# Kernel optimization log

Hardware: AMD Instinct MI355X
Metric: run time of the kernel (lower is better)

Reference implementation:

```python
import jax, jax.numpy as jnp
import numpy as np

D_MODEL = 1024
N_HEADS = 16
D_HEAD = D_MODEL // N_HEADS
ROPE_BASE = 10000.0


def setup_inputs() -> dict:
    key = jax.random.key(0)
    k1, k2, k3, k4, k5 = jax.random.split(key, 5)
    std = 0.02 / np.sqrt(2 * 12)  # scaled_xavier with n_layers=12
    x = jax.random.normal(k1, (2, 2048, D_MODEL), dtype=jnp.float32)
    qkv_w = jax.random.normal(k2, (3 * D_MODEL, D_MODEL), dtype=jnp.float32) * std
    qkv_b = jnp.zeros((3 * D_MODEL,), dtype=jnp.float32)
    proj_w = jax.random.normal(k3, (D_MODEL, D_MODEL), dtype=jnp.float32) * std
    proj_b = jnp.zeros((D_MODEL,), dtype=jnp.float32)
    return {"x": x, "qkv_w": qkv_w, "qkv_b": qkv_b, "proj_w": proj_w, "proj_b": proj_b}


def _rope_cos_sin(seq_len, dtype):
    inv_freq = 1.0 / (ROPE_BASE ** (jnp.arange(0, D_HEAD, 2, dtype=jnp.float32) / D_HEAD))
    t = jnp.arange(seq_len, dtype=jnp.float32)
    freqs = jnp.einsum("t,d->td", t, inv_freq)          # [S, Dh/2]
    freqs = jnp.concatenate([freqs, freqs], axis=-1)      # [S, Dh]
    return jnp.cos(freqs).astype(dtype), jnp.sin(freqs).astype(dtype)


def _rotate_half(x):
    x1, x2 = jnp.split(x, 2, axis=-1)
    return jnp.concatenate([-x2, x1], axis=-1)


def reference(x, qkv_w, qkv_b, proj_w, proj_b):
    B, S, D = x.shape
    H, Dh = N_HEADS, D_HEAD
    scale = 1.0 / np.sqrt(Dh)

    qkv = x @ qkv_w.T + qkv_b                              # [B, S, 3D]
    qkv = qkv.reshape(B, S, 3, H, Dh)
    q = jnp.transpose(qkv[:, :, 0], (0, 2, 1, 3))          # [B, H, S, Dh]
    k = jnp.transpose(qkv[:, :, 1], (0, 2, 1, 3))
    v = jnp.transpose(qkv[:, :, 2], (0, 2, 1, 3))

    cos, sin = _rope_cos_sin(S, x.dtype)                   # [S, Dh]
    q = q * cos + _rotate_half(q) * sin
    k = k * cos + _rotate_half(k) * sin

    scores = jnp.einsum("bhsd,bhtd->bhst", q, k) * scale   # [B, H, S, S]
    causal = jnp.triu(jnp.ones((S, S), dtype=bool), k=1)
    neg = jnp.finfo(scores.dtype).min
    scores = jnp.where(causal[None, None], neg, scores)

    probs = jax.nn.softmax(scores, axis=-1)
    ctx = jnp.einsum("bhst,bhtd->bhsd", probs, v)          # [B, H, S, Dh]
    out = jnp.transpose(ctx, (0, 2, 1, 3)).reshape(B, S, D)
    out = out @ proj_w.T + proj_b
    return out
```

## Files before the change

kernel.cpp:

```cpp
#include <hip/hip_runtime.h>
#include <hip/hip_bf16.h>

#define BATCH 2
#define SEQ   2048
#define DMODEL 1024
#define NHEADS 16
#define DHEAD  64
#define MTOT   (BATCH * SEQ)
#define QKSTR  2048

typedef __attribute__((ext_vector_type(8))) short bf16x8;
typedef __attribute__((ext_vector_type(4))) float f32x4;

__device__ __forceinline__ void glds16(const void* g, void* l)
{
    __builtin_amdgcn_global_load_lds(
        (const __attribute__((address_space(1))) unsigned int*)g,
        (__attribute__((address_space(3))) unsigned int*)l, 16, 0, 0);
}

__device__ __forceinline__ unsigned cvt_pk_bf16(float lo, float hi)
{
    unsigned r;
    asm("v_cvt_pk_bf16_f32 %0, %1, %2" : "=v"(r) : "v"(lo), "v"(hi));
    return r;
}

__global__ void cast_all_kernel(
    const float* __restrict__ a, __hip_bfloat16* __restrict__ oa, int na4,
    const float* __restrict__ b, __hip_bfloat16* __restrict__ ob, int nb4,
    const float* __restrict__ c, __hip_bfloat16* __restrict__ oc, int nc4)
{
    int i = blockIdx.x * blockDim.x + threadIdx.x;
    const float* src; __hip_bfloat16* dst; int j = i;
    if (j < na4) { src = a; dst = oa; }
    else {
        j -= na4;
        if (j < nb4) { src = b; dst = ob; }
        else {
            j -= nb4;
            if (j >= nc4) return;
            src = c; dst = oc;
        }
    }
    float4 v = ((const float4*)src)[j];
    __hip_bfloat16 tmp[4];
    tmp[0] = __float2bfloat16(v.x);
    tmp[1] = __float2bfloat16(v.y);
    tmp[2] = __float2bfloat16(v.z);
    tmp[3] = __float2bfloat16(v.w);
    *(uint2*)(dst + 4 * (size_t)j) = *(const uint2*)tmp;
}

#define GBK 64

__device__ __forceinline__ void store_out(float* p, float v) { *p = v; }
__device__ __forceinline__ void store_out(__hip_bfloat16* p, float v) { *p = __float2bfloat16(v); }

template <typename OutT, int MODE, int TM, int TN, int MINW>
__global__ __launch_bounds__(256, MINW) void gemm_bias_kernel(
    const __hip_bfloat16* __restrict__ A, const __hip_bfloat16* __restrict__ W,
    const float* __restrict__ bias, OutT* __restrict__ out,
    __hip_bfloat16* __restrict__ vtg,
    int M, int N, int K)
{
    const int MI = TM / 32;
    const int NI = TN / 32;
    const int bm = blockIdx.x * TM;
    const int bn = blockIdx.y * TN;
    const int tid = threadIdx.x;
    const int wave = tid >> 6;
    const int lane = tid & 63;
    const int quad = lane >> 4;
    const int l16 = lane & 15;
    const int wm = (wave & 1) * (TM / 2);
    const int wn = (wave >> 1) * (TN / 2);

    __shared__ __hip_bfloat16 As[TM * GBK];
    __shared__ __hip_bfloat16 Bs[TN * GBK];

    f32x4 acc[MI][NI] = {};

    const int srow = lane >> 3;
    const int gc8 = (((lane & 7) ^ srow)) * 8;

    for (int kt = 0; kt < K; kt += GBK) {
#pragma unroll
        for (int t = 0; t < MI; t++) {
            int i = wave * MI + t;
            glds16(A + (size_t)(bm + i * 8 + srow) * K + kt + gc8, As + i * 512);
        }
#pragma unroll
        for (int t = 0; t < NI; t++) {
            int i = wave * NI + t;
            glds16(W + (size_t)(bn + i * 8 + srow) * K + kt + gc8, Bs + i * 512);
        }
        __syncthreads();

#pragma unroll
        for (int kk = 0; kk < 2; kk++) {
            bf16x8 af[MI], bfr[NI];
#pragma unroll
            for (int i = 0; i < MI; i++) {
                int ra = wm + i * 16 + l16;
                af[i] = *(const bf16x8*)(As + ra * 64 + (((kk << 2) + quad) ^ (ra & 7)) * 8);
            }
#pragma unroll
            for (int i = 0; i < NI; i++) {
                int rb = wn + i * 16 + l16;
                bfr[i] = *(const bf16x8*)(Bs + rb * 64 + (((kk << 2) + quad) ^ (rb & 7)) * 8);
            }
#pragma unroll
            for (int mi = 0; mi < MI; mi++)
#pragma unroll
                for (int ni = 0; ni < NI; ni++)
                    acc[mi][ni] = __builtin_amdgcn_mfma_f32_16x16x32_bf16(
                        af[mi], bfr[ni], acc[mi][ni], 0, 0, 0);
        }
        __syncthreads();
    }

    if (MODE == 1 && (bn + wn) < 2 * DMODEL) {
#pragma unroll
        for (int ni = 0; ni < 2; ni++) {
            int col = bn + wn + ni * 16 + l16;
            int i32 = col & 31;
            float invf = exp2f(-13.287712379549449f * (float)i32 * (1.0f / 32.0f));
            float b1 = bias[col], b2 = bias[col + 32];
#pragma unroll
            for (int mi = 0; mi < MI; mi++) {
#pragma unroll
                for (int r = 0; r < 4; r++) {
                    int row = bm + wm + mi * 16 + quad * 4 + r;
                    int s = row & (SEQ - 1);
                    float ang = (float)s * invf;
                    float sn, cs;
                    __sincosf(ang, &sn, &cs);
                    float x1 = acc[mi][ni][r] + b1;
                    float x2 = acc[mi][ni + 2][r] + b2;
                    store_out(&out[(size_t)row * QKSTR + col], x1 * cs - x2 * sn);
                    store_out(&out[(size_t)row * QKSTR + col + 32], x2 * cs + x1 * sn);
                }
            }
        }
    } else if (MODE == 1) {
#pragma unroll
        for (int ni = 0; ni < NI; ni++) {
            int colg = bn + wn + ni * 16 + l16;
            int vcol = colg - 2 * DMODEL;
            int hh = vcol >> 6, dh = vcol & 63;
            float bv = bias[colg];
#pragma unroll
            for (int mi = 0; mi < MI; mi++) {
                int row0 = bm + wm + mi * 16 + quad * 4;
                int bb = row0 >> 11;
                int ss = row0 & (SEQ - 1);
                __hip_bfloat16 tmp[4];
#pragma unroll
                for (int r = 0; r < 4; r++)
                    tmp[r] = __float2bfloat16(acc[mi][ni][r] + bv);
                *(uint2*)(vtg + (((size_t)bb * NHEADS + hh) * DHEAD + dh) * SEQ + ss) =
                    *(uint2*)tmp;
            }
        }
    } else {
#pragma unroll
        for (int mi = 0; mi < MI; mi++)
#pragma unroll
            for (int ni = 0; ni < NI; ni++) {
                int col = bn + wn + ni * 16 + l16;
                float bv = bias[col];
#pragma unroll
                for (int r = 0; r < 4; r++) {
                    int row = bm + wm + mi * 16 + quad * 4 + r;
                    store_out(&out[(size_t)row * N + col], acc[mi][ni][r] + bv);
                }
            }
    }
}

__global__ __launch_bounds__(256, 4) void flash_attn_mfma_kernel(
    const __hip_bfloat16* __restrict__ qkb,
    const __hip_bfloat16* __restrict__ vtg,
    __hip_bfloat16* __restrict__ ctx)
{
    const int bh = blockIdx.x;
    const int b = bh >> 4, h = bh & 15;
    const int qt = 31 - blockIdx.y;
    const int tid = threadIdx.x;
    const int w = tid >> 6;
    const int lane = tid & 63;
    const int quad = lane >> 4;
    const int l16 = lane & 15;

    __shared__ alignas(16) __hip_bfloat16 Ks[2][64 * 64];
    __shared__ alignas(16) __hip_bfloat16 Vt[2][64 * 64];
    __shared__ alignas(16) __hip_bfloat16 Ps[64 * 64];

    const __hip_bfloat16* qbase = qkb + (size_t)b * SEQ * QKSTR + h * DHEAD;
    const __hip_bfloat16* kbase = qbase + DMODEL;
    const __hip_bfloat16* vbase = vtg + (size_t)bh * DHEAD * SEQ;

    const __hip_bfloat16* qrow = qbase + (size_t)(qt * 64 + w * 16 + l16) * QKSTR;
    bf16x8 qf0 = *(const bf16x8*)(qrow + quad * 8);
    bf16x8 qf1 = *(const bf16x8*)(qrow + 32 + quad * 8);

    const int srow = lane >> 3;
    const int gc8 = ((lane & 7) ^ srow) * 8;
    const __hip_bfloat16* kg = kbase + (size_t)(w * 16 + srow) * QKSTR + gc8;
    const __hip_bfloat16* vg = vbase + (size_t)(w * 16 + srow) * SEQ + gc8;

    const int xr = l16 & 7;
    const int fo0 = l16 * 64 + ((quad ^ xr) << 3);
    const int fo1 = l16 * 64 + (((4 + quad) ^ xr) << 3);
    const int pband = w * 16;
    char* const psb = (char*)Ps;
    const int pr0 = (pband + l16) * 128 + ((quad ^ xr) << 4);
    const int pr1 = (pband + l16) * 128 + (((4 + quad) ^ xr) << 4);
    int pwc[4];
#pragma unroll
    for (int nt = 0; nt < 4; nt++)
        pwc[nt] = (pband + l16) * 128 +
                  ((((nt << 1) + (quad >> 1)) ^ xr) << 4) + (quad & 1) * 8;

    const short onev = (l16 == 0) ? (short)0x3F80 : (short)0;
    const bf16x8 ones = {onev, onev, onev, onev, onev, onev, onev, onev};

    f32x4 oacc[5] = {};

    auto stage = [&](int t, int buf) {
        const __hip_bfloat16* kt_ = kg + (size_t)t * 64 * QKSTR;
        const __hip_bfloat16* vt_ = vg + t * 64;
        glds16(kt_,              &Ks[buf][w * 1024]);
        glds16(kt_ + 8 * QKSTR,  &Ks[buf][w * 1024 + 512]);
        glds16(vt_,              &Vt[buf][w * 1024]);
        glds16(vt_ + 8 * SEQ,    &Vt[buf][w * 1024 + 512]);
    };

    stage(0, 0);

    for (int jt = 0; jt <= qt; jt++) {
        __syncthreads();
        const int cur = jt & 1;
        if (jt < qt) stage(jt + 1, cur ^ 1);
        const __hip_bfloat16* ks = Ks[cur];
        const __hip_bfloat16* vs = Vt[cur];

        f32x4 s4[4] = {};
        __builtin_amdgcn_s_setprio(1);
#pragma unroll
        for (int nt = 0; nt < 4; nt++)
            s4[nt] = __builtin_amdgcn_mfma_f32_16x16x32_bf16(
                *(const bf16x8*)(ks + nt * 1024 + fo0), qf0, s4[nt], 0, 0, 0);
#pragma unroll
        for (int nt = 0; nt < 4; nt++)
            s4[nt] = __builtin_amdgcn_mfma_f32_16x16x32_bf16(
                *(const bf16x8*)(ks + nt * 1024 + fo1), qf1, s4[nt], 0, 0, 0);
        __builtin_amdgcn_s_setprio(0);

        const bool diag = (jt == qt);
        const int qq = w * 16 + l16;
#pragma unroll
        for (int nt = 0; nt < 4; nt++) {
            float p0 = exp2f(s4[nt][0] * 0.1803368801f);
            float p1 = exp2f(s4[nt][1] * 0.1803368801f);
            float p2 = exp2f(s4[nt][2] * 0.1803368801f);
            float p3 = exp2f(s4[nt][3] * 0.1803368801f);
            if (diag) {
                int k0 = nt * 16 + quad * 4;
                p0 = (k0 + 0 <= qq) ? p0 : 0.f;
                p1 = (k0 + 1 <= qq) ? p1 : 0.f;
                p2 = (k0 + 2 <= qq) ? p2 : 0.f;
                p3 = (k0 + 3 <= qq) ? p3 : 0.f;
            }
            uint2 pv;
            pv.x = cvt_pk_bf16(p0, p1);
            pv.y = cvt_pk_bf16(p2, p3);
            *(uint2*)(psb + pwc[nt]) = pv;
        }

        bf16x8 pf0 = *(const bf16x8*)(psb + pr0);
        bf16x8 pf1 = *(const bf16x8*)(psb + pr1);
        __builtin_amdgcn_s_setprio(1);
#pragma unroll
        for (int dt = 0; dt < 4; dt++)
            oacc[dt] = __builtin_amdgcn_mfma_f32_16x16x32_bf16(
                pf0, *(const bf16x8*)(vs + dt * 1024 + fo0), oacc[dt], 0, 0, 0);
        oacc[4] = __builtin_amdgcn_mfma_f32_16x16x32_bf16(pf0, ones, oacc[4], 0, 0, 0);
#pragma unroll
        for (int dt = 0; dt < 4; dt++)
            oacc[dt] = __builtin_amdgcn_mfma_f32_16x16x32_bf16(
                pf1, *(const bf16x8*)(vs + dt * 1024 + fo1), oacc[dt], 0, 0, 0);
        oacc[4] = __builtin_amdgcn_mfma_f32_16x16x32_bf16(pf1, ones, oacc[4], 0, 0, 0);
        __builtin_amdgcn_s_setprio(0);
    }

#pragma unroll
    for (int r = 0; r < 4; r++) {
        float lv = __shfl(oacc[4][r], lane & 48);
        float il = 1.0f / lv;
        int qg = qt * 64 + w * 16 + quad * 4 + r;
        __hip_bfloat16* op = ctx + (((size_t)b * SEQ + qg) * NHEADS + h) * DHEAD + l16;
#pragma unroll
        for (int dt = 0; dt < 4; dt++)
            op[dt * 16] = __float2bfloat16(oacc[dt][r] * il);
    }
}

extern "C" void kernel_launch(void* const* d_in, const int* in_sizes, int n_in,
                              void* d_out, int out_size, void* d_ws, size_t ws_size,
                              hipStream_t stream)
{
    const float* x      = (const float*)d_in[0];
    const float* qkv_w  = (const float*)d_in[1];
    const float* qkv_b  = (const float*)d_in[2];
    const float* proj_w = (const float*)d_in[3];
    const float* proj_b = (const float*)d_in[4];
    float* out = (float*)d_out;

    char* w = (char*)d_ws;
    __hip_bfloat16* qkb = (__hip_bfloat16*)w;  w += (size_t)MTOT * QKSTR * 2;
    __hip_bfloat16* vtg = (__hip_bfloat16*)w;  w += (size_t)MTOT * DMODEL * 2;
    __hip_bfloat16* ctx = (__hip_bfloat16*)w;  w += (size_t)MTOT * DMODEL * 2;
    __hip_bfloat16* xb  = (__hip_bfloat16*)w;  w += (size_t)MTOT * DMODEL * 2;
    __hip_bfloat16* wqk = (__hip_bfloat16*)w;  w += (size_t)3 * DMODEL * DMODEL * 2;
    __hip_bfloat16* wpr = (__hip_bfloat16*)w;

    const int na4 = MTOT * DMODEL / 4;
    const int nb4 = 3 * DMODEL * DMODEL / 4;
    const int nc4 = DMODEL * DMODEL / 4;

    cast_all_kernel<<<(na4 + nb4 + nc4 + 255) / 256, 256, 0, stream>>>(
        x, xb, na4, qkv_w, wqk, nb4, proj_w, wpr, nc4);

    gemm_bias_kernel<__hip_bfloat16, 1, 128, 128, 3>
        <<<dim3(MTOT / 128, (3 * DMODEL) / 128), 256, 0, stream>>>(
        xb, wqk, qkv_b, qkb, vtg, MTOT, 3 * DMODEL, DMODEL);

    flash_attn_mfma_kernel<<<dim3(BATCH * NHEADS, 32), 256, 0, stream>>>(qkb, vtg, ctx);

    gemm_bias_kernel<float, 0, 64, 128, 6>
        <<<dim3(MTOT / 64, DMODEL / 128), 256, 0, stream>>>(
        ctx, wpr, proj_b, out, nullptr, MTOT, DMODEL, DMODEL);
}
```

Before: 168.6 us.

## Balance causal attention work by pairing query tiles and splitting keys

Each attention block now does a fixed 16–17 key-tile iterations instead of 1–32. A role-0 block handles a short query tile qa and then the first part of a long tile qb. A role-1 block handles the rest of qb. The partial unnormalized outputs and row sums for the long tiles go to fp32 scratch buffers, and a new finalize kernel combines them. This removes the causal load imbalance and tail effect, at the cost of an extra kernel launch and extra global traffic for the fp32 partials. The o0 buffer reuses the xb workspace, which is safe only because xb is no longer needed after the QKV GEMM.

```diff
diff --git a/kernel.cpp b/kernel.cpp
--- a/kernel.cpp
+++ b/kernel.cpp
@@ -182,11 +182,16 @@
 __global__ __launch_bounds__(256, 4) void flash_attn_mfma_kernel(
     const __hip_bfloat16* __restrict__ qkb,
     const __hip_bfloat16* __restrict__ vtg,
-    __hip_bfloat16* __restrict__ ctx)
+    __hip_bfloat16* __restrict__ ctx,
+    float* __restrict__ o0, float* __restrict__ o1,
+    float* __restrict__ l0, float* __restrict__ l1)
 {
     const int bh = blockIdx.x;
     const int b = bh >> 4, h = bh & 15;
-    const int qt = 31 - blockIdx.y;
+    const int yy = blockIdx.y;
+    const int role = yy >> 4;
+    const int y = yy & 15;
+    const int qa = y, qb = 31 - y;
     const int tid = threadIdx.x;
     const int w = tid >> 6;
     const int lane = tid & 63;
@@ -201,9 +206,13 @@
     const __hip_bfloat16* kbase = qbase + DMODEL;
     const __hip_bfloat16* vbase = vtg + (size_t)bh * DHEAD * SEQ;
 
-    const __hip_bfloat16* qrow = qbase + (size_t)(qt * 64 + w * 16 + l16) * QKSTR;
+    const int qt0 = role ? qb : qa;
+    const __hip_bfloat16* qrow = qbase + (size_t)(qt0 * 64 + w * 16 + l16) * QKSTR;
     bf16x8 qf0 = *(const bf16x8*)(qrow + quad * 8);
     bf16x8 qf1 = *(const bf16x8*)(qrow + 32 + quad * 8);
+    const __hip_bfloat16* qrows = qbase + (size_t)(qb * 64 + w * 16 + l16) * QKSTR;
+    bf16x8 qs0 = *(const bf16x8*)(qrows + quad * 8);
+    bf16x8 qs1 = *(const bf16x8*)(qrows + 32 + quad * 8);
 
     const int srow = lane >> 3;
     const int gc8 = ((lane & 7) ^ srow) * 8;
@@ -237,12 +246,28 @@
         glds16(vt_ + 8 * SEQ,    &Vt[buf][w * 1024 + 512]);
     };
 
-    stage(0, 0);
-
-    for (int jt = 0; jt <= qt; jt++) {
+    auto kof = [&](int n) { return role ? n : (n <= qa ? n : n + 15 - qa); };
+
+    auto write_ctx = [&](int qt) {
+#pragma unroll
+        for (int r = 0; r < 4; r++) {
+            float lv = __shfl(oacc[4][r], lane & 48);
+            float il = 1.0f / lv;
+            int qg = qt * 64 + w * 16 + quad * 4 + r;
+            __hip_bfloat16* op = ctx + (((size_t)b * SEQ + qg) * NHEADS + h) * DHEAD + l16;
+#pragma unroll
+            for (int dt = 0; dt < 4; dt++)
+                op[dt * 16] = __float2bfloat16(oacc[dt][r] * il);
+        }
+    };
+
+    const int nit = 17 - role;
+    stage(kof(0), 0);
+
+    for (int n = 0; n < nit; n++) {
         __syncthreads();
-        const int cur = jt & 1;
-        if (jt < qt) stage(jt + 1, cur ^ 1);
+        const int cur = n & 1;
+        if (n + 1 < nit) stage(kof(n + 1), cur ^ 1);
         const __hip_bfloat16* ks = Ks[cur];
         const __hip_bfloat16* vs = Vt[cur];
 
@@ -258,7 +283,7 @@
                 *(const bf16x8*)(ks + nt * 1024 + fo1), qf1, s4[nt], 0, 0, 0);
         __builtin_amdgcn_s_setprio(0);
 
-        const bool diag = (jt == qt);
+        const bool diag = (!role) && (n == qa || n == 16);
         const int qq = w * 16 + l16;
 #pragma unroll
         for (int nt = 0; nt < 4; nt++) {
@@ -293,18 +318,50 @@
                 pf1, *(const bf16x8*)(vs + dt * 1024 + fo1), oacc[dt], 0, 0, 0);
         oacc[4] = __builtin_amdgcn_mfma_f32_16x16x32_bf16(pf1, ones, oacc[4], 0, 0, 0);
         __builtin_amdgcn_s_setprio(0);
+
+        if (!role && n == qa) {
+            write_ctx(qa);
+#pragma unroll
+            for (int i = 0; i < 5; i++) oacc[i] = f32x4{0.f, 0.f, 0.f, 0.f};
+            qf0 = qs0; qf1 = qs1;
+        }
     }
 
+    float* ob = role ? o1 : o0;
+    float* lb = role ? l1 : l0;
+    const int rbase = bh * 1024 + (qb - 16) * 64 + w * 16;
 #pragma unroll
     for (int r = 0; r < 4; r++) {
-        float lv = __shfl(oacc[4][r], lane & 48);
-        float il = 1.0f / lv;
-        int qg = qt * 64 + w * 16 + quad * 4 + r;
-        __hip_bfloat16* op = ctx + (((size_t)b * SEQ + qg) * NHEADS + h) * DHEAD + l16;
+        int rr = rbase + quad * 4 + r;
 #pragma unroll
         for (int dt = 0; dt < 4; dt++)
-            op[dt * 16] = __float2bfloat16(oacc[dt][r] * il);
+            ob[(size_t)rr * 64 + dt * 16 + l16] = oacc[dt][r];
+        if (l16 == 0) lb[rr] = oacc[4][r];
     }
+}
+
+__global__ void attn_finalize_kernel(
+    const float* __restrict__ o0, const float* __restrict__ o1,
+    const float* __restrict__ l0, const float* __restrict__ l1,
+    __hip_bfloat16* __restrict__ ctx)
+{
+    int t = blockIdx.x * blockDim.x + threadIdx.x;
+    int dh4 = t & 15;
+    int row = t >> 4;
+    int bh = row >> 10;
+    int qrow = row & 1023;
+    int b = bh >> 4, h = bh & 15;
+    float il = 1.0f / (l0[row] + l1[row]);
+    float4 a = ((const float4*)(o0 + (size_t)row * 64))[dh4];
+    float4 c = ((const float4*)(o1 + (size_t)row * 64))[dh4];
+    __hip_bfloat16 tmp[4];
+    tmp[0] = __float2bfloat16((a.x + c.x) * il);
+    tmp[1] = __float2bfloat16((a.y + c.y) * il);
+    tmp[2] = __float2bfloat16((a.z + c.z) * il);
+    tmp[3] = __float2bfloat16((a.w + c.w) * il);
+    int s = 1024 + qrow;
+    *(uint2*)(ctx + (((size_t)b * SEQ + s) * NHEADS + h) * DHEAD + dh4 * 4) =
+        *(uint2*)tmp;
 }
 
 extern "C" void kernel_launch(void* const* d_in, const int* in_sizes, int n_in,
@@ -324,7 +381,11 @@
     __hip_bfloat16* ctx = (__hip_bfloat16*)w;  w += (size_t)MTOT * DMODEL * 2;
     __hip_bfloat16* xb  = (__hip_bfloat16*)w;  w += (size_t)MTOT * DMODEL * 2;
     __hip_bfloat16* wqk = (__hip_bfloat16*)w;  w += (size_t)3 * DMODEL * DMODEL * 2;
-    __hip_bfloat16* wpr = (__hip_bfloat16*)w;
+    __hip_bfloat16* wpr = (__hip_bfloat16*)w;  w += (size_t)DMODEL * DMODEL * 2;
+    float* o0 = (float*)xb;
+    float* o1 = (float*)w;  w += (size_t)32 * 1024 * 64 * 4;
+    float* l0 = (float*)w;  w += (size_t)32 * 1024 * 4;
+    float* l1 = (float*)w;
 
     const int na4 = MTOT * DMODEL / 4;
     const int nb4 = 3 * DMODEL * DMODEL / 4;
@@ -337,7 +398,10 @@
         <<<dim3(MTOT / 128, (3 * DMODEL) / 128), 256, 0, stream>>>(
         xb, wqk, qkv_b, qkb, vtg, MTOT, 3 * DMODEL, DMODEL);
 
-    flash_attn_mfma_kernel<<<dim3(BATCH * NHEADS, 32), 256, 0, stream>>>(qkb, vtg, ctx);
+    flash_attn_mfma_kernel<<<dim3(BATCH * NHEADS, 32), 256, 0, stream>>>(
+        qkb, vtg, ctx, o0, o1, l0, l1);
+
+    attn_finalize_kernel<<<2048, 256, 0, stream>>>(o0, o1, l0, l1, ctx);
 
     gemm_bias_kernel<float, 0, 64, 128, 6>
         <<<dim3(MTOT / 64, DMODEL / 128), 256, 0, stream>>>(
```

Measured after the change: 176.1 us. 1.04x slower.

## Feed softmax probabilities directly into 16x16x16 MFMA, drop LDS P staging

Applied to the files above, without the earlier changes.

Removes the shared-memory round trip for the probability tile. The S accumulator layout of each 16-column block is reused directly as the A operand of the 16x16x16 bf16 MFMA, reading V fragments with matching swizzled offsets. Dropping the Ps buffer frees LDS, so launch bounds are raised to 5 blocks per CU. Query tiles are also reordered to interleave long and short causal tiles for better load balance. The trade is twice as many smaller MFMAs for the PV product and possibly more register pressure under the tighter occupancy bound.

```diff
diff --git a/kernel.cpp b/kernel.cpp
--- a/kernel.cpp
+++ b/kernel.cpp
@@ -10,6 +10,7 @@
 #define QKSTR  2048
 
 typedef __attribute__((ext_vector_type(8))) short bf16x8;
+typedef __attribute__((ext_vector_type(4))) short bf16x4;
 typedef __attribute__((ext_vector_type(4))) float f32x4;
 
 __device__ __forceinline__ void glds16(const void* g, void* l)
@@ -179,14 +180,15 @@
     }
 }
 
-__global__ __launch_bounds__(256, 4) void flash_attn_mfma_kernel(
+__global__ __launch_bounds__(256, 5) void flash_attn_mfma_kernel(
     const __hip_bfloat16* __restrict__ qkb,
     const __hip_bfloat16* __restrict__ vtg,
     __hip_bfloat16* __restrict__ ctx)
 {
     const int bh = blockIdx.x;
     const int b = bh >> 4, h = bh & 15;
-    const int qt = 31 - blockIdx.y;
+    const int y = blockIdx.y;
+    const int qt = (y < 8) ? 31 - y : (y < 16) ? y - 8 : (y < 24) ? 39 - y : y - 16;
     const int tid = threadIdx.x;
     const int w = tid >> 6;
     const int lane = tid & 63;
@@ -195,7 +197,6 @@
 
     __shared__ alignas(16) __hip_bfloat16 Ks[2][64 * 64];
     __shared__ alignas(16) __hip_bfloat16 Vt[2][64 * 64];
-    __shared__ alignas(16) __hip_bfloat16 Ps[64 * 64];
 
     const __hip_bfloat16* qbase = qkb + (size_t)b * SEQ * QKSTR + h * DHEAD;
     const __hip_bfloat16* kbase = qbase + DMODEL;
@@ -213,18 +214,16 @@
     const int xr = l16 & 7;
     const int fo0 = l16 * 64 + ((quad ^ xr) << 3);
     const int fo1 = l16 * 64 + (((4 + quad) ^ xr) << 3);
-    const int pband = w * 16;
-    char* const psb = (char*)Ps;
-    const int pr0 = (pband + l16) * 128 + ((quad ^ xr) << 4);
-    const int pr1 = (pband + l16) * 128 + (((4 + quad) ^ xr) << 4);
-    int pwc[4];
+    int vbse[4], vchk[4];
+#pragma unroll
+    for (int dt = 0; dt < 4; dt++)
+        vbse[dt] = (dt * 16 + l16) * 64 + (quad & 1) * 4;
 #pragma unroll
     for (int nt = 0; nt < 4; nt++)
-        pwc[nt] = (pband + l16) * 128 +
-                  ((((nt << 1) + (quad >> 1)) ^ xr) << 4) + (quad & 1) * 8;
-
-    const short onev = (l16 == 0) ? (short)0x3F80 : (short)0;
-    const bf16x8 ones = {onev, onev, onev, onev, onev, onev, onev, onev};
+        vchk[nt] = (((nt << 1) + (quad >> 1)) ^ xr) << 3;
+
+    const short ov = (l16 == 0) ? (short)0x3F80 : (short)0;
+    const bf16x4 ones4 = {ov, ov, ov, ov};
 
     f32x4 oacc[5] = {};
 
@@ -273,26 +272,20 @@
                 p2 = (k0 + 2 <= qq) ? p2 : 0.f;
                 p3 = (k0 + 3 <= qq) ? p3 : 0.f;
             }
-            uint2 pv;
-            pv.x = cvt_pk_bf16(p0, p1);
-            pv.y = cvt_pk_bf16(p2, p3);
-            *(uint2*)(psb + pwc[nt]) = pv;
-        }
-
-        bf16x8 pf0 = *(const bf16x8*)(psb + pr0);
-        bf16x8 pf1 = *(const bf16x8*)(psb + pr1);
-        __builtin_amdgcn_s_setprio(1);
-#pragma unroll
-        for (int dt = 0; dt < 4; dt++)
-            oacc[dt] = __builtin_amdgcn_mfma_f32_16x16x32_bf16(
-                pf0, *(const bf16x8*)(vs + dt * 1024 + fo0), oacc[dt], 0, 0, 0);
-        oacc[4] = __builtin_amdgcn_mfma_f32_16x16x32_bf16(pf0, ones, oacc[4], 0, 0, 0);
-#pragma unroll
-        for (int dt = 0; dt < 4; dt++)
-            oacc[dt] = __builtin_amdgcn_mfma_f32_16x16x32_bf16(
-                pf1, *(const bf16x8*)(vs + dt * 1024 + fo1), oacc[dt], 0, 0, 0);
-        oacc[4] = __builtin_amdgcn_mfma_f32_16x16x32_bf16(pf1, ones, oacc[4], 0, 0, 0);
-        __builtin_amdgcn_s_setprio(0);
+            union { unsigned u[2]; bf16x4 v; } pu;
+            pu.u[0] = cvt_pk_bf16(p0, p1);
+            pu.u[1] = cvt_pk_bf16(p2, p3);
+            const bf16x4 pa = pu.v;
+
+            __builtin_amdgcn_s_setprio(1);
+#pragma unroll
+            for (int dt = 0; dt < 4; dt++)
+                oacc[dt] = __builtin_amdgcn_mfma_f32_16x16x16bf16_1k(
+                    pa, *(const bf16x4*)(vs + vbse[dt] + vchk[nt]), oacc[dt], 0, 0, 0);
+            oacc[4] = __builtin_amdgcn_mfma_f32_16x16x16bf16_1k(
+                pa, ones4, oacc[4], 0, 0, 0);
+            __builtin_amdgcn_s_setprio(0);
+        }
     }
 
 #pragma unroll
```

Measured after the change: 174.1 us. 1.03x slower.
